# Optimization experiments

Hardware: AMD Instinct MI355X
Metric: run time of the kernel (lower is better)

Reference implementation:

```python
import jax, jax.numpy as jnp
import numpy as np

N = 100000
E = 1600000

def gcn_conv(x, w, b, row, col, ew, n):
    # PyG GCNConv: linear transform, add self-loops (weight 1), symmetric
    # degree normalization with edge weights, scatter-sum to destinations.
    h = x @ w  # [N, out]
    loop = jnp.arange(n)
    row2 = jnp.concatenate([row, loop])
    col2 = jnp.concatenate([col, loop])
    ew2 = jnp.concatenate([ew, jnp.ones((n,), x.dtype)])
    deg = jax.ops.segment_sum(ew2, col2, num_segments=n)
    dinv = jnp.where(deg > 0, jax.lax.rsqrt(deg), jnp.zeros_like(deg))
    norm = dinv[row2] * ew2 * dinv[col2]  # [E+N]
    msg = h[row2] * norm[:, None]  # [E+N, out]
    out = jax.ops.segment_sum(msg, col2, num_segments=n)
    return out + b


def setup_inputs() -> dict:
    key = jax.random.key(0)
    ks = jax.random.split(key, 8)
    x = jax.random.normal(ks[0], (N, 256), dtype=jnp.float32)
    edge_index = jax.random.randint(ks[1], (2, E), 0, N, dtype=jnp.int64)
    edge_attr = jax.random.uniform(ks[2], (E,), dtype=jnp.float32)
    w_dense = jax.random.normal(ks[3], (256, 256), dtype=jnp.float32) * 0.05
    b_dense = jnp.zeros((256,), jnp.float32)
    w_enc = jax.random.normal(ks[4], (256, 256), dtype=jnp.float32) * 0.05
    b_enc = jnp.zeros((256,), jnp.float32)
    w_mu = jax.random.normal(ks[5], (256, 128), dtype=jnp.float32) * 0.05
    b_mu = jnp.zeros((128,), jnp.float32)
    w_logstd = jax.random.normal(ks[6], (256, 128), dtype=jnp.float32) * 0.05
    b_logstd = jnp.zeros((128,), jnp.float32)
    return {"x": x, "edge_index": edge_index, "edge_attr": edge_attr,
            "w_dense": w_dense, "b_dense": b_dense, "w_enc": w_enc, "b_enc": b_enc,
            "w_mu": w_mu, "b_mu": b_mu, "w_logstd": w_logstd, "b_logstd": b_logstd}


def reference(x, edge_index, edge_attr, w_dense, b_dense, w_enc, b_enc, w_mu, b_mu, w_logstd, b_logstd):
    row, col = edge_index[0], edge_index[1]
    h = jax.nn.relu(x @ w_dense + b_dense)  # dense + relu; dropout is identity in eval
    # enc_layer=2 -> encoder[:-1] applies exactly one hidden GCNConv
    h = gcn_conv(h, w_enc, b_enc, row, col, edge_attr, N)
    mu = gcn_conv(h, w_mu, b_mu, row, col, edge_attr, N)
    logstd = gcn_conv(h, w_logstd, b_logstd, row, col, edge_attr, N)
    return (mu, logstd)
```

## Files before the change

### kernel.cpp

```cpp
#include <hip/hip_runtime.h>


typedef short bf16x8 __attribute__((ext_vector_type(8)));
typedef float f32x4 __attribute__((ext_vector_type(4)));

static __device__ __forceinline__ unsigned int f2bf(float f) {
    unsigned int u = __float_as_uint(f);
    return ((u + 0x7fffu + ((u >> 16) & 1u)) >> 16) & 0xffffu;
}
static __device__ __forceinline__ float bf2f(unsigned int us) {
    return __uint_as_float(us << 16);
}

static __device__ __forceinline__ void load_lds16(const void* g, void* l) {
    __builtin_amdgcn_global_load_lds(
        (const __attribute__((address_space(1))) unsigned int*)g,
        (__attribute__((address_space(3))) unsigned int*)l, 16, 0, 0);
}

#define FIXSCALE 8388608.0f


__global__ __launch_bounds__(256) void init_kernel(unsigned long long* acc, int n) {
    int i = blockIdx.x * 256 + threadIdx.x;
    if (i < n) acc[i] = 0ull;
}

__global__ __launch_bounds__(256) void edge_pack_kernel(const int* __restrict__ col,
                                                        const float* __restrict__ ew,
                                                        unsigned long long* __restrict__ acc,
                                                        unsigned int* __restrict__ rank, int E) {
    int e = blockIdx.x * 256 + threadIdx.x;
    if (e < E) {
        int c = col[e];
        unsigned long long pk = (1ull << 32) |
                                (unsigned long long)(unsigned int)(ew[e] * FIXSCALE + 0.5f);
        unsigned long long old = atomicAdd(&acc[c], pk);
        rank[e] = (unsigned int)(old >> 32);
    }
}

__global__ __launch_bounds__(256) void dinv_kernel(const unsigned long long* __restrict__ acc,
                                                   float* __restrict__ dinv, int n) {
    int i = blockIdx.x * 256 + threadIdx.x;
    if (i < n) {
        float deg = 1.0f + (float)(unsigned int)acc[i] * (1.0f / FIXSCALE);
        dinv[i] = rsqrtf(deg);
    }
}

__global__ __launch_bounds__(1024) void scanA_kernel(const unsigned long long* __restrict__ acc,
                                                     int* __restrict__ offsets,
                                                     int* __restrict__ bsum, int n) {
    __shared__ int wsum[16];
    int tid = threadIdx.x, lane = tid & 63, wv = tid >> 6;
    int i = blockIdx.x * 1024 + tid;
    int v = (i < n) ? (int)(acc[i] >> 32) : 0;
    int s = v;
#pragma unroll
    for (int off = 1; off < 64; off <<= 1) {
        int t = __shfl_up(s, off, 64);
        if (lane >= off) s += t;
    }
    if (lane == 63) wsum[wv] = s;
    __syncthreads();
    if (wv == 0 && lane < 16) {
        int w = wsum[lane];
        int ss = w;
#pragma unroll
        for (int off = 1; off < 16; off <<= 1) {
            int t = __shfl_up(ss, off, 64);
            if (lane >= off) ss += t;
        }
        wsum[lane] = ss - w;
        if (lane == 15) bsum[blockIdx.x] = ss;
    }
    __syncthreads();
    if (i < n) offsets[i] = wsum[wv] + s - v;
}

__global__ __launch_bounds__(128) void scanB_kernel(int* __restrict__ bsum, int nb,
                                                    int* __restrict__ offsets, int n) {
    __shared__ int w0tot;
    int tid = threadIdx.x, lane = tid & 63, wv = tid >> 6;
    int v = (tid < nb) ? bsum[tid] : 0;
    int s = v;
#pragma unroll
    for (int off = 1; off < 64; off <<= 1) {
        int t = __shfl_up(s, off, 64);
        if (lane >= off) s += t;
    }
    if (wv == 0 && lane == 63) w0tot = s;
    __syncthreads();
    int excl = s - v + (wv ? w0tot : 0);
    if (tid < nb) bsum[tid] = excl;
    if (tid == nb - 1) offsets[n] = excl + v;
}

__global__ __launch_bounds__(256) void scanC_kernel(int* __restrict__ offsets,
                                                    const int* __restrict__ bsum, int n) {
    int i = blockIdx.x * 256 + threadIdx.x;
    if (i < n) offsets[i] += bsum[i >> 10];
}

__global__ __launch_bounds__(256) void fill2_kernel(const int* __restrict__ row,
                                                    const int* __restrict__ col,
                                                    const float* __restrict__ ew,
                                                    const unsigned int* __restrict__ rank,
                                                    const int* __restrict__ offsets,
                                                    const float* __restrict__ dinv,
                                                    uint2* __restrict__ edges, int E) {
    int e = blockIdx.x * 256 + threadIdx.x;
    if (e < E) {
        int c = col[e];
        int r = row[e];
        int pos = offsets[c] + (int)rank[e];
        uint2 p;
        p.x = (unsigned int)r;
        p.y = __float_as_uint(dinv[r] * ew[e]);
        edges[pos] = p;
    }
}

__global__ __launch_bounds__(256) void cvt_frag_kernel(const float* __restrict__ x,
                                                       unsigned short* __restrict__ Af, int n) {
    int g = blockIdx.x * 256 + threadIdx.x;
    int c = g >> 6, lane = g & 63;
    if (c >= n) return;
    float4 v = ((const float4*)x)[(size_t)c * 64 + lane];
    uint2 w;
    w.x = f2bf(v.x) | (f2bf(v.y) << 16);
    w.y = f2bf(v.z) | (f2bf(v.w) << 16);
    int T = c >> 4, l = c & 15;
    size_t idx8 = (size_t)T * 1024 + (size_t)((lane >> 3)) * 128 + ((lane >> 1) & 3) * 32 + l * 2 + (lane & 1);
    ((uint2*)Af)[idx8] = w;
}

__global__ __launch_bounds__(256) void splitw_kernel(const float* __restrict__ W, int M,
                                                     unsigned short* __restrict__ hi,
                                                     unsigned short* __restrict__ lo) {
    int idx = blockIdx.x * 256 + threadIdx.x;
    if (idx < M * 256) {
        int c = idx >> 8, k = idx & 255;
        float w = W[k * M + c];
        unsigned int h = f2bf(w);
        float r = w - bf2f(h);
        int T = c >> 4, l = c & 15, K = k >> 5, q = (k >> 3) & 3, j = k & 7;
        size_t o = (size_t)(T * 8 + K) * 512 + q * 128 + l * 8 + j;
        hi[o] = (unsigned short)h;
        lo[o] = (unsigned short)f2bf(r);
    }
}

__global__ __launch_bounds__(256) void bcat_kernel(const float* __restrict__ a,
                                                   const float* __restrict__ b,
                                                   float* __restrict__ o) {
    int t = threadIdx.x;
    o[t] = (t < 128) ? a[t] : b[t - 128];
}

#define ACC8(qv, uv)                                      \
    do {                                                  \
        float w_ = __uint_as_float((qv).y);               \
        a0 += w_ * __uint_as_float((uv).x << 16);         \
        a1 += w_ * __uint_as_float((uv).x & 0xffff0000u); \
        a2 += w_ * __uint_as_float((uv).y << 16);         \
        a3 += w_ * __uint_as_float((uv).y & 0xffff0000u); \
        a4 += w_ * __uint_as_float((uv).z << 16);         \
        a5 += w_ * __uint_as_float((uv).z & 0xffff0000u); \
        a6 += w_ * __uint_as_float((uv).w << 16);         \
        a7 += w_ * __uint_as_float((uv).w & 0xffff0000u); \
    } while (0)

__global__ __launch_bounds__(256) void spmm_kernel(const unsigned short* __restrict__ h,
                                                   const uint2* __restrict__ edges,
                                                   const int* __restrict__ offsets,
                                                   const float* __restrict__ dinv,
                                                   unsigned short* __restrict__ outf, int n) {
    int wave = threadIdx.x >> 6;
    int lane = threadIdx.x & 63;
    int half = lane >> 5, hl = lane & 31;
    int c = blockIdx.x * 4 + wave;
    if (c >= n) return;
    const uint4* __restrict__ h4 = (const uint4*)h;
    float di = dinv[c];
    int beg = __builtin_amdgcn_readfirstlane(offsets[c]);
    int end = __builtin_amdgcn_readfirstlane(offsets[c + 1]);
    int d = end - beg;
    int elim = beg + (d & ~1);

    float a0 = 0.f, a1 = 0.f, a2 = 0.f, a3 = 0.f;
    float a4 = 0.f, a5 = 0.f, a6 = 0.f, a7 = 0.f;

    int e = beg;
    for (; e + 8 <= elim; e += 8) {
        uint2 q0 = edges[e + 0 + half];
        uint2 q1 = edges[e + 2 + half];
        uint2 q2 = edges[e + 4 + half];
        uint2 q3 = edges[e + 6 + half];
        uint4 u0 = h4[(size_t)q0.x * 32 + hl];
        uint4 u1 = h4[(size_t)q1.x * 32 + hl];
        uint4 u2 = h4[(size_t)q2.x * 32 + hl];
        uint4 u3 = h4[(size_t)q3.x * 32 + hl];
        ACC8(q0, u0);
        ACC8(q1, u1);
        ACC8(q2, u2);
        ACC8(q3, u3);
    }
    for (; e < elim; e += 2) {
        uint2 q = edges[e + half];
        uint4 u = h4[(size_t)q.x * 32 + hl];
        ACC8(q, u);
    }
    {
        uint2 qf;
        qf.x = (unsigned int)c;
        qf.y = half ? 0u : __float_as_uint(di);
        if (half && (d & 1)) qf = edges[end - 1];
        uint4 uf = h4[(size_t)qf.x * 32 + hl];
        ACC8(qf, uf);
    }

    a0 += __shfl_xor(a0, 32);
    a1 += __shfl_xor(a1, 32);
    a2 += __shfl_xor(a2, 32);
    a3 += __shfl_xor(a3, 32);
    a4 += __shfl_xor(a4, 32);
    a5 += __shfl_xor(a5, 32);
    a6 += __shfl_xor(a6, 32);
    a7 += __shfl_xor(a7, 32);

    if (half == 0) {
        uint4 wv;
        wv.x = f2bf(di * a0) | (f2bf(di * a1) << 16);
        wv.y = f2bf(di * a2) | (f2bf(di * a3) << 16);
        wv.z = f2bf(di * a4) | (f2bf(di * a5) << 16);
        wv.w = f2bf(di * a6) | (f2bf(di * a7) << 16);
        int T = c >> 4, l = c & 15;
        size_t o16 = ((size_t)T * 8 + (hl >> 2)) * 512 + (size_t)(hl & 3) * 128 + (size_t)l * 8;
        *(uint4*)(outf + o16) = wv;
    }
}

__global__ __launch_bounds__(256) void mfma_gemm_kernel(const unsigned short* __restrict__ Af,
                                                        const unsigned short* __restrict__ Wh,
                                                        const unsigned short* __restrict__ Wl,
                                                        const float* __restrict__ bias,
                                                        void* __restrict__ outp,
                                                        int n, int M, int flags) {
    __shared__ short lds[2][12288];
    int tid = threadIdx.x, lane = tid & 63, wave = tid >> 6;
    int wr = wave & 1, wc = wave >> 1;
    int l16 = lane & 15, quad = lane >> 4;
    int T0 = blockIdx.x * 8;
    int Tc0 = blockIdx.y * 8;

    f32x4 acc[4][4];
#pragma unroll
    for (int i = 0; i < 4; ++i)
#pragma unroll
        for (int j = 0; j < 4; ++j) acc[i][j] = (f32x4)0.0f;

    auto stage = [&](int b, int K) {
#pragma unroll
        for (int j = 0; j < 6; ++j) {
            int cid = wave * 6 + j;
            const unsigned short* g;
            if (cid < 8)       g = Af + ((size_t)(T0 + cid) * 8 + K) * 512;
            else if (cid < 16) g = Wh + ((size_t)(Tc0 + cid - 8) * 8 + K) * 512;
            else               g = Wl + ((size_t)(Tc0 + cid - 16) * 8 + K) * 512;
            load_lds16(g + (size_t)lane * 8, &lds[b][cid * 512]);
        }
    };

    stage(0, 0);
    __syncthreads();

    for (int K = 0; K < 8; ++K) {
        int cur = K & 1;
        if (K < 7) stage(cur ^ 1, K + 1);
        bf16x8 af[4], bh[4], bl[4];
#pragma unroll
        for (int t = 0; t < 4; ++t) {
            af[t] = *(const bf16x8*)(&lds[cur][0] + (4 * wr + t) * 512 + lane * 8);
            bh[t] = *(const bf16x8*)(&lds[cur][0] + 4096 + (4 * wc + t) * 512 + lane * 8);
            bl[t] = *(const bf16x8*)(&lds[cur][0] + 8192 + (4 * wc + t) * 512 + lane * 8);
        }
#pragma unroll
        for (int rt = 0; rt < 4; ++rt)
#pragma unroll
            for (int ct = 0; ct < 4; ++ct) {
                acc[rt][ct] = __builtin_amdgcn_mfma_f32_16x16x32_bf16(af[rt], bh[ct], acc[rt][ct], 0, 0, 0);
                acc[rt][ct] = __builtin_amdgcn_mfma_f32_16x16x32_bf16(af[rt], bl[ct], acc[rt][ct], 0, 0, 0);
            }
        if (K < 7) __syncthreads();
    }

    int relu = flags & 1, obf = flags & 2, dual = flags & 4;
    int r0 = T0 * 16, c0 = Tc0 * 16;
#pragma unroll
    for (int ct = 0; ct < 4; ++ct) {
        int col = c0 + 64 * wc + 16 * ct + l16;
        float b = bias[col];
#pragma unroll
        for (int rt = 0; rt < 4; ++rt) {
            int rbase = r0 + 64 * wr + 16 * rt + quad * 4;
#pragma unroll
            for (int i = 0; i < 4; ++i) {
                int r = rbase + i;
                if (r < n) {
                    float v = acc[rt][ct][i] + b;
                    if (relu) v = fmaxf(v, 0.0f);
                    if (dual)
                        ((float*)outp)[(size_t)(col >> 7) * ((size_t)n * 128) + (size_t)r * 128 + (col & 127)] = v;
                    else if (obf)
                        ((unsigned short*)outp)[(size_t)r * M + col] = (unsigned short)f2bf(v);
                    else
                        ((float*)outp)[(size_t)r * M + col] = v;
                }
            }
        }
    }
}


extern "C" void kernel_launch(void* const* d_in, const int* in_sizes, int n_in,
                              void* d_out, int out_size, void* d_ws, size_t ws_size,
                              hipStream_t stream) {
    const float* x        = (const float*)d_in[0];
    const int*   ei       = (const int*)d_in[1];
    const float* ea       = (const float*)d_in[2];
    const float* w_dense  = (const float*)d_in[3];
    const float* b_dense  = (const float*)d_in[4];
    const float* w_enc    = (const float*)d_in[5];
    const float* b_enc    = (const float*)d_in[6];
    const float* w_mu     = (const float*)d_in[7];
    const float* b_mu     = (const float*)d_in[8];
    const float* w_logstd = (const float*)d_in[9];
    const float* b_logstd = (const float*)d_in[10];

    const int n = in_sizes[0] / 256;
    const int E = in_sizes[2];
    const int* row = ei;
    const int* col = ei + E;

    char* ws = (char*)d_ws;
    size_t off = 0;
    auto alloc = [&](size_t bytes) -> void* {
        void* p = ws + off;
        off = (off + bytes + 255) & ~(size_t)255;
        return p;
    };
    const int nTile = (n + 127) / 128;
    const int nTpad = nTile * 8;
    unsigned long long* acc = (unsigned long long*)alloc((size_t)n * 8);
    float* dinv   = (float*)alloc((size_t)n * 4);
    int*   offs   = (int*)alloc((size_t)(n + 1) * 4);
    int*   bsum   = (int*)alloc(128 * 4);
    unsigned int* rank = (unsigned int*)alloc((size_t)E * 4);
    uint2* edges  = (uint2*)alloc((size_t)E * 8);
    unsigned short* Af   = (unsigned short*)alloc((size_t)nTpad * 8192);
    unsigned short* wd_h = (unsigned short*)alloc(256 * 256 * 2);
    unsigned short* wd_l = (unsigned short*)alloc(256 * 256 * 2);
    unsigned short* we_h = (unsigned short*)alloc(256 * 256 * 2);
    unsigned short* we_l = (unsigned short*)alloc(256 * 256 * 2);
    unsigned short* wf_h = (unsigned short*)alloc(256 * 256 * 2);
    unsigned short* wf_l = (unsigned short*)alloc(256 * 256 * 2);
    float*          bcat = (float*)alloc(256 * 4);
    (void)ws_size;

    unsigned short* h1b = (unsigned short*)d_out;
    unsigned short* h0b = (unsigned short*)d_out + (size_t)n * 256;

    int nb_n = (n + 255) / 256;
    int nb_e = (E + 255) / 256;
    int nb_s = (n + 1023) / 1024;

    init_kernel<<<nb_n, 256, 0, stream>>>(acc, n);
    edge_pack_kernel<<<nb_e, 256, 0, stream>>>(col, ea, acc, rank, E);
    dinv_kernel<<<nb_n, 256, 0, stream>>>(acc, dinv, n);
    scanA_kernel<<<nb_s, 1024, 0, stream>>>(acc, offs, bsum, n);
    scanB_kernel<<<1, 128, 0, stream>>>(bsum, nb_s, offs, n);
    scanC_kernel<<<nb_n, 256, 0, stream>>>(offs, bsum, n);
    fill2_kernel<<<nb_e, 256, 0, stream>>>(row, col, ea, rank, offs, dinv, edges, E);

    cvt_frag_kernel<<<(n * 64 + 255) / 256, 256, 0, stream>>>(x, Af, n);
    splitw_kernel<<<256, 256, 0, stream>>>(w_dense, 256, wd_h, wd_l);
    splitw_kernel<<<256, 256, 0, stream>>>(w_enc, 256, we_h, we_l);
    splitw_kernel<<<128, 256, 0, stream>>>(w_mu, 128, wf_h, wf_l);
    splitw_kernel<<<128, 256, 0, stream>>>(w_logstd, 128, wf_h + 32768, wf_l + 32768);
    bcat_kernel<<<1, 256, 0, stream>>>(b_mu, b_logstd, bcat);

    mfma_gemm_kernel<<<dim3(nTile, 2), 256, 0, stream>>>(Af, wd_h, wd_l, b_dense, h0b, n, 256, 1 | 2);
    spmm_kernel<<<(n + 3) / 4, 256, 0, stream>>>(h0b, edges, offs, dinv, Af, n);
    mfma_gemm_kernel<<<dim3(nTile, 2), 256, 0, stream>>>(Af, we_h, we_l, b_enc, h1b, n, 256, 2);
    spmm_kernel<<<(n + 3) / 4, 256, 0, stream>>>(h1b, edges, offs, dinv, Af, n);
    mfma_gemm_kernel<<<dim3(nTile, 2), 256, 0, stream>>>(Af, wf_h, wf_l, bcat, d_out, n, 128, 4);
}
```

Baseline: 764.4 us.

## Split SpMM aggregation into two column-half passes with four edges per wave

The gather-aggregate kernel now handles 128 of the 256 feature columns per launch, with each wave using four 16-lane groups that each process a different edge. It is launched twice per layer, once per column half. The aim is to shrink the gathered working set per pass (64 of the 128 bf16 bytes per row, 6.4 MB instead of 12.8 MB for h) so it fits better in L2/LLC, and to issue more independent edge gathers at once. The cost is reading the edge list and offsets twice, an extra shuffle reduction step, and an additional kernel launch.

```diff
diff --git a/kernel.cpp b/kernel.cpp
--- a/kernel.cpp
+++ b/kernel.cpp
@@ -176,68 +176,72 @@
                                                    const uint2* __restrict__ edges,
                                                    const int* __restrict__ offsets,
                                                    const float* __restrict__ dinv,
-                                                   unsigned short* __restrict__ outf, int n) {
+                                                   unsigned short* __restrict__ outf,
+                                                   int n, int colbase) {
     int wave = threadIdx.x >> 6;
     int lane = threadIdx.x & 63;
-    int half = lane >> 5, hl = lane & 31;
+    int quarter = lane >> 4, ql = lane & 15;
     int c = blockIdx.x * 4 + wave;
     if (c >= n) return;
     const uint4* __restrict__ h4 = (const uint4*)h;
+    int cq = colbase >> 3;
     float di = dinv[c];
     int beg = __builtin_amdgcn_readfirstlane(offsets[c]);
     int end = __builtin_amdgcn_readfirstlane(offsets[c + 1]);
     int d = end - beg;
-    int elim = beg + (d & ~1);
+    int elim = beg + (d & ~3);
 
     float a0 = 0.f, a1 = 0.f, a2 = 0.f, a3 = 0.f;
     float a4 = 0.f, a5 = 0.f, a6 = 0.f, a7 = 0.f;
 
     int e = beg;
-    for (; e + 8 <= elim; e += 8) {
-        uint2 q0 = edges[e + 0 + half];
-        uint2 q1 = edges[e + 2 + half];
-        uint2 q2 = edges[e + 4 + half];
-        uint2 q3 = edges[e + 6 + half];
-        uint4 u0 = h4[(size_t)q0.x * 32 + hl];
-        uint4 u1 = h4[(size_t)q1.x * 32 + hl];
-        uint4 u2 = h4[(size_t)q2.x * 32 + hl];
-        uint4 u3 = h4[(size_t)q3.x * 32 + hl];
+    for (; e + 16 <= elim; e += 16) {
+        uint2 q0 = edges[e + 0 + quarter];
+        uint2 q1 = edges[e + 4 + quarter];
+        uint2 q2 = edges[e + 8 + quarter];
+        uint2 q3 = edges[e + 12 + quarter];
+        uint4 u0 = h4[(size_t)q0.x * 32 + cq + ql];
+        uint4 u1 = h4[(size_t)q1.x * 32 + cq + ql];
+        uint4 u2 = h4[(size_t)q2.x * 32 + cq + ql];
+        uint4 u3 = h4[(size_t)q3.x * 32 + cq + ql];
         ACC8(q0, u0);
         ACC8(q1, u1);
         ACC8(q2, u2);
         ACC8(q3, u3);
     }
-    for (; e < elim; e += 2) {
-        uint2 q = edges[e + half];
-        uint4 u = h4[(size_t)q.x * 32 + hl];
+    for (; e < elim; e += 4) {
+        uint2 q = edges[e + quarter];
+        uint4 u = h4[(size_t)q.x * 32 + cq + ql];
         ACC8(q, u);
     }
     {
+        int rt = d & 3;
         uint2 qf;
         qf.x = (unsigned int)c;
-        qf.y = half ? 0u : __float_as_uint(di);
-        if (half && (d & 1)) qf = edges[end - 1];
-        uint4 uf = h4[(size_t)qf.x * 32 + hl];
+        qf.y = quarter ? 0u : __float_as_uint(di);
+        if (quarter > 0 && (quarter - 1) < rt) qf = edges[end - rt + quarter - 1];
+        uint4 uf = h4[(size_t)qf.x * 32 + cq + ql];
         ACC8(qf, uf);
     }
 
-    a0 += __shfl_xor(a0, 32);
-    a1 += __shfl_xor(a1, 32);
-    a2 += __shfl_xor(a2, 32);
-    a3 += __shfl_xor(a3, 32);
-    a4 += __shfl_xor(a4, 32);
-    a5 += __shfl_xor(a5, 32);
-    a6 += __shfl_xor(a6, 32);
-    a7 += __shfl_xor(a7, 32);
-
-    if (half == 0) {
+    a0 += __shfl_xor(a0, 32); a0 += __shfl_xor(a0, 16);
+    a1 += __shfl_xor(a1, 32); a1 += __shfl_xor(a1, 16);
+    a2 += __shfl_xor(a2, 32); a2 += __shfl_xor(a2, 16);
+    a3 += __shfl_xor(a3, 32); a3 += __shfl_xor(a3, 16);
+    a4 += __shfl_xor(a4, 32); a4 += __shfl_xor(a4, 16);
+    a5 += __shfl_xor(a5, 32); a5 += __shfl_xor(a5, 16);
+    a6 += __shfl_xor(a6, 32); a6 += __shfl_xor(a6, 16);
+    a7 += __shfl_xor(a7, 32); a7 += __shfl_xor(a7, 16);
+
+    if (quarter == 0) {
         uint4 wv;
         wv.x = f2bf(di * a0) | (f2bf(di * a1) << 16);
         wv.y = f2bf(di * a2) | (f2bf(di * a3) << 16);
         wv.z = f2bf(di * a4) | (f2bf(di * a5) << 16);
         wv.w = f2bf(di * a6) | (f2bf(di * a7) << 16);
         int T = c >> 4, l = c & 15;
-        size_t o16 = ((size_t)T * 8 + (hl >> 2)) * 512 + (size_t)(hl & 3) * 128 + (size_t)l * 8;
+        size_t o16 = ((size_t)T * 8 + (colbase >> 5) + (ql >> 2)) * 512 +
+                     (size_t)(ql & 3) * 128 + (size_t)l * 8;
         *(uint4*)(outf + o16) = wv;
     }
 }
@@ -375,6 +379,7 @@
     int nb_n = (n + 255) / 256;
     int nb_e = (E + 255) / 256;
     int nb_s = (n + 1023) / 1024;
+    int nb_sp = (n + 3) / 4;
 
     init_kernel<<<nb_n, 256, 0, stream>>>(acc, n);
     edge_pack_kernel<<<nb_e, 256, 0, stream>>>(col, ea, acc, rank, E);
@@ -392,8 +397,10 @@
     bcat_kernel<<<1, 256, 0, stream>>>(b_mu, b_logstd, bcat);
 
     mfma_gemm_kernel<<<dim3(nTile, 2), 256, 0, stream>>>(Af, wd_h, wd_l, b_dense, h0b, n, 256, 1 | 2);
-    spmm_kernel<<<(n + 3) / 4, 256, 0, stream>>>(h0b, edges, offs, dinv, Af, n);
+    spmm_kernel<<<nb_sp, 256, 0, stream>>>(h0b, edges, offs, dinv, Af, n, 0);
+    spmm_kernel<<<nb_sp, 256, 0, stream>>>(h0b, edges, offs, dinv, Af, n, 128);
     mfma_gemm_kernel<<<dim3(nTile, 2), 256, 0, stream>>>(Af, we_h, we_l, b_enc, h1b, n, 256, 2);
-    spmm_kernel<<<(n + 3) / 4, 256, 0, stream>>>(h1b, edges, offs, dinv, Af, n);
+    spmm_kernel<<<nb_sp, 256, 0, stream>>>(h1b, edges, offs, dinv, Af, n, 0);
+    spmm_kernel<<<nb_sp, 256, 0, stream>>>(h1b, edges, offs, dinv, Af, n, 128);
     mfma_gemm_kernel<<<dim3(nTile, 2), 256, 0, stream>>>(Af, wf_h, wf_l, bcat, d_out, n, 128, 4);
 }
```

Result: no change. 774.0 us (+1.3%).

## Fuse edge degree-packing atomics into first dense GEMM launch for overlap

Applied to the files above, without the earlier changes.

Merges the edge_pack atomic degree/rank pass into the first MFMA GEMM kernel as extra blocks, so the memory/atomic-bound edge work runs concurrently with the compute-bound dense layer. The graph preprocessing chain (dinv, scans, fill) moves after this combined launch. The combined kernel inherits the GEMM's LDS allocation for the edge blocks, which may limit how many edge blocks are resident at once.

```diff
diff --git a/kernel.cpp b/kernel.cpp
--- a/kernel.cpp
+++ b/kernel.cpp
@@ -24,20 +24,6 @@
 __global__ __launch_bounds__(256) void init_kernel(unsigned long long* acc, int n) {
     int i = blockIdx.x * 256 + threadIdx.x;
     if (i < n) acc[i] = 0ull;
-}
-
-__global__ __launch_bounds__(256) void edge_pack_kernel(const int* __restrict__ col,
-                                                        const float* __restrict__ ew,
-                                                        unsigned long long* __restrict__ acc,
-                                                        unsigned int* __restrict__ rank, int E) {
-    int e = blockIdx.x * 256 + threadIdx.x;
-    if (e < E) {
-        int c = col[e];
-        unsigned long long pk = (1ull << 32) |
-                                (unsigned long long)(unsigned int)(ew[e] * FIXSCALE + 0.5f);
-        unsigned long long old = atomicAdd(&acc[c], pk);
-        rank[e] = (unsigned int)(old >> 32);
-    }
 }
 
 __global__ __launch_bounds__(256) void dinv_kernel(const unsigned long long* __restrict__ acc,
@@ -242,18 +228,18 @@
     }
 }
 
-__global__ __launch_bounds__(256) void mfma_gemm_kernel(const unsigned short* __restrict__ Af,
-                                                        const unsigned short* __restrict__ Wh,
-                                                        const unsigned short* __restrict__ Wl,
-                                                        const float* __restrict__ bias,
-                                                        void* __restrict__ outp,
-                                                        int n, int M, int flags) {
-    __shared__ short lds[2][12288];
+static __device__ __forceinline__ void gemm_body(const unsigned short* __restrict__ Af,
+                                                 const unsigned short* __restrict__ Wh,
+                                                 const unsigned short* __restrict__ Wl,
+                                                 const float* __restrict__ bias,
+                                                 void* __restrict__ outp,
+                                                 int n, int M, int flags,
+                                                 int bx, int by, short* lds ) {
     int tid = threadIdx.x, lane = tid & 63, wave = tid >> 6;
     int wr = wave & 1, wc = wave >> 1;
     int l16 = lane & 15, quad = lane >> 4;
-    int T0 = blockIdx.x * 8;
-    int Tc0 = blockIdx.y * 8;
+    int T0 = bx * 8;
+    int Tc0 = by * 8;
 
     f32x4 acc[4][4];
 #pragma unroll
@@ -269,7 +255,7 @@
             if (cid < 8)       g = Af + ((size_t)(T0 + cid) * 8 + K) * 512;
             else if (cid < 16) g = Wh + ((size_t)(Tc0 + cid - 8) * 8 + K) * 512;
             else               g = Wl + ((size_t)(Tc0 + cid - 16) * 8 + K) * 512;
-            load_lds16(g + (size_t)lane * 8, &lds[b][cid * 512]);
+            load_lds16(g + (size_t)lane * 8, lds + b * 12288 + cid * 512);
         }
     };
 
@@ -282,9 +268,9 @@
         bf16x8 af[4], bh[4], bl[4];
 #pragma unroll
         for (int t = 0; t < 4; ++t) {
-            af[t] = *(const bf16x8*)(&lds[cur][0] + (4 * wr + t) * 512 + lane * 8);
-            bh[t] = *(const bf16x8*)(&lds[cur][0] + 4096 + (4 * wc + t) * 512 + lane * 8);
-            bl[t] = *(const bf16x8*)(&lds[cur][0] + 8192 + (4 * wc + t) * 512 + lane * 8);
+            af[t] = *(const bf16x8*)(lds + cur * 12288 + (4 * wr + t) * 512 + lane * 8);
+            bh[t] = *(const bf16x8*)(lds + cur * 12288 + 4096 + (4 * wc + t) * 512 + lane * 8);
+            bl[t] = *(const bf16x8*)(lds + cur * 12288 + 8192 + (4 * wc + t) * 512 + lane * 8);
         }
 #pragma unroll
         for (int rt = 0; rt < 4; ++rt)
@@ -319,6 +305,43 @@
                         ((float*)outp)[(size_t)r * M + col] = v;
                 }
             }
+        }
+    }
+}
+
+__global__ __launch_bounds__(256) void mfma_gemm_kernel(const unsigned short* __restrict__ Af,
+                                                        const unsigned short* __restrict__ Wh,
+                                                        const unsigned short* __restrict__ Wl,
+                                                        const float* __restrict__ bias,
+                                                        void* __restrict__ outp,
+                                                        int n, int M, int flags) {
+    __shared__ short lds[2 * 12288];
+    gemm_body(Af, Wh, Wl, bias, outp, n, M, flags, blockIdx.x, blockIdx.y, lds);
+}
+
+__global__ __launch_bounds__(256) void gemm_pack_kernel(const unsigned short* __restrict__ Af,
+                                                        const unsigned short* __restrict__ Wh,
+                                                        const unsigned short* __restrict__ Wl,
+                                                        const float* __restrict__ bias,
+                                                        void* __restrict__ outp,
+                                                        int n, int M, int flags,
+                                                        int nGemm, int nTile,
+                                                        const int* __restrict__ col,
+                                                        const float* __restrict__ ew,
+                                                        unsigned long long* __restrict__ acc,
+                                                        unsigned int* __restrict__ rank, int E) {
+    __shared__ short lds[2 * 12288];
+    int b = blockIdx.x;
+    if (b < nGemm) {
+        gemm_body(Af, Wh, Wl, bias, outp, n, M, flags, b % nTile, b / nTile, lds);
+    } else {
+        int e = (b - nGemm) * 256 + threadIdx.x;
+        if (e < E) {
+            int c = col[e];
+            unsigned long long pk = (1ull << 32) |
+                                    (unsigned long long)(unsigned int)(ew[e] * FIXSCALE + 0.5f);
+            unsigned long long old = atomicAdd(&acc[c], pk);
+            rank[e] = (unsigned int)(old >> 32);
         }
     }
 }
@@ -375,15 +398,9 @@
     int nb_n = (n + 255) / 256;
     int nb_e = (E + 255) / 256;
     int nb_s = (n + 1023) / 1024;
+    int nGemm = nTile * 2;
 
     init_kernel<<<nb_n, 256, 0, stream>>>(acc, n);
-    edge_pack_kernel<<<nb_e, 256, 0, stream>>>(col, ea, acc, rank, E);
-    dinv_kernel<<<nb_n, 256, 0, stream>>>(acc, dinv, n);
-    scanA_kernel<<<nb_s, 1024, 0, stream>>>(acc, offs, bsum, n);
-    scanB_kernel<<<1, 128, 0, stream>>>(bsum, nb_s, offs, n);
-    scanC_kernel<<<nb_n, 256, 0, stream>>>(offs, bsum, n);
-    fill2_kernel<<<nb_e, 256, 0, stream>>>(row, col, ea, rank, offs, dinv, edges, E);
-
     cvt_frag_kernel<<<(n * 64 + 255) / 256, 256, 0, stream>>>(x, Af, n);
     splitw_kernel<<<256, 256, 0, stream>>>(w_dense, 256, wd_h, wd_l);
     splitw_kernel<<<256, 256, 0, stream>>>(w_enc, 256, we_h, we_l);
@@ -391,7 +408,16 @@
     splitw_kernel<<<128, 256, 0, stream>>>(w_logstd, 128, wf_h + 32768, wf_l + 32768);
     bcat_kernel<<<1, 256, 0, stream>>>(b_mu, b_logstd, bcat);
 
-    mfma_gemm_kernel<<<dim3(nTile, 2), 256, 0, stream>>>(Af, wd_h, wd_l, b_dense, h0b, n, 256, 1 | 2);
+    gemm_pack_kernel<<<nGemm + nb_e, 256, 0, stream>>>(Af, wd_h, wd_l, b_dense, h0b,
+                                                       n, 256, 1 | 2, nGemm, nTile,
+                                                       col, ea, acc, rank, E);
+
+    dinv_kernel<<<nb_n, 256, 0, stream>>>(acc, dinv, n);
+    scanA_kernel<<<nb_s, 1024, 0, stream>>>(acc, offs, bsum, n);
+    scanB_kernel<<<1, 128, 0, stream>>>(bsum, nb_s, offs, n);
+    scanC_kernel<<<nb_n, 256, 0, stream>>>(offs, bsum, n);
+    fill2_kernel<<<nb_e, 256, 0, stream>>>(row, col, ea, rank, offs, dinv, edges, E);
+
     spmm_kernel<<<(n + 3) / 4, 256, 0, stream>>>(h0b, edges, offs, dinv, Af, n);
     mfma_gemm_kernel<<<dim3(nTile, 2), 256, 0, stream>>>(Af, we_h, we_l, b_enc, h1b, n, 256, 2);
     spmm_kernel<<<(n + 3) / 4, 256, 0, stream>>>(h1b, edges, offs, dinv, Af, n);
```

Measured after the change: 748.9 us. -2.0%, faster.
